# Performance work log

Measured on AMD Instinct MI355X. Metric: run time of the kernel, lower is better.

Reference implementation:

```python
import math
import jax, jax.numpy as jnp
import numpy as np

B, S, D, H = 2, 2048, 2048, 16
HD = D // H  # 128
EPS = 1e-5


def setup_inputs() -> dict:
    key = jax.random.key(0)
    ks = jax.random.split(key, 7)
    x = jax.random.normal(ks[0], (B, S, D), jnp.float32)
    # RoPE tables: (seqlen, head_dim//2)
    theta = 10000.0
    inv_freq = 1.0 / (theta ** (np.arange(0, HD, 2, dtype=np.float32) / HD))
    t = np.arange(S, dtype=np.float32)
    freqs = np.outer(t, inv_freq)  # (S, HD//2)
    freqs_cos = jnp.asarray(np.cos(freqs), jnp.float32)
    freqs_sin = jnp.asarray(np.sin(freqs), jnp.float32)
    sc = 0.02
    wq = jax.random.normal(ks[1], (D, D), jnp.float32) * sc  # stored (in, out)
    wk = jax.random.normal(ks[2], (D, D), jnp.float32) * sc
    wv = jax.random.normal(ks[3], (D, D), jnp.float32) * sc
    wu = jax.random.normal(ks[4], (D, D), jnp.float32) * sc
    wo = jax.random.normal(ks[5], (D, D), jnp.float32) * sc
    norm_w = jnp.ones((D,), jnp.float32)
    return {"x": x, "freqs_cos": freqs_cos, "freqs_sin": freqs_sin,
            "wq": wq, "wk": wk, "wv": wv, "wu": wu, "wo": wo, "norm_w": norm_w}


def _rope(t, cos, sin):
    # t: (B, S, H, HD); cos/sin: (S, HD//2)
    tr = t.reshape(t.shape[:-1] + (-1, 2))
    r, i = tr[..., 0], tr[..., 1]
    c = cos[None, :, None, :]
    s = sin[None, :, None, :]
    out_r = r * c - i * s
    out_i = r * s + i * c
    return jnp.stack([out_r, out_i], axis=-1).reshape(t.shape)


def reference(x, freqs_cos, freqs_sin, wq, wk, wv, wu, wo, norm_w):
    b, s, d = x.shape
    h = jax.nn.silu(x)  # pre-projection SiLU on the input
    q = (h @ wq).reshape(b, s, H, HD)
    k = (h @ wk).reshape(b, s, H, HD)
    v = (h @ wv).reshape(b, s, H, HD)
    u = h @ wu  # reshape->transpose->flatten in original is identity on (b,s,d)
    q = _rope(q, freqs_cos, freqs_sin)
    k = _rope(k, freqs_cos, freqs_sin)
    # scores: (b, H, s, s)
    scores = jnp.einsum('bqhd,bkhd->bhqk', q, k) / math.sqrt(HD)
    causal = jnp.tril(jnp.ones((s, s), bool))  # mask!=0 positions zeroed; silu(0)=0
    scores = jnp.where(causal[None, None], jax.nn.silu(scores), 0.0)
    out = jnp.einsum('bhqk,bkhd->bqhd', scores, v).reshape(b, s, d)
    # RMSNorm
    out = out * jax.lax.rsqrt(jnp.mean(out * out, axis=-1, keepdims=True) + EPS)
    out = out * norm_w
    out = out * u
    return out @ wo
```

## Files before the change

### kernel.cpp

```cpp
#include <hip/hip_runtime.h>
#include <hip/hip_bf16.h>
#include <cstdint>

typedef __attribute__((ext_vector_type(8))) short bf16x8;
typedef __attribute__((ext_vector_type(4))) float f32x4;
typedef unsigned short u16;

constexpr int B = 2, S = 2048, D = 2048, H = 16, HD = 128;
constexpr int M = B * S;
constexpr int NQKU = 6144;
constexpr int ATT_LD = 3072;
constexpr float SCALE = 0.08838834764831845f;

static __device__ __forceinline__ float b2f(u16 u) {
    union { float f; uint32_t i; } v; v.i = ((uint32_t)u) << 16; return v.f;
}
static __device__ __forceinline__ u16 f2b(float f) {
    union { float f; uint32_t i; } v; v.f = f;
    uint32_t x = v.i;
    return (u16)((x + 0x7FFFu + ((x >> 16) & 1u)) >> 16);
}

__device__ __forceinline__ void gll16(const void* g, void* l) {
    __builtin_amdgcn_global_load_lds(
        (const __attribute__((address_space(1))) uint32_t*)g,
        (__attribute__((address_space(3))) uint32_t*)l, 16, 0, 0);
}

#define BAR() do { asm volatile("" ::: "memory"); __builtin_amdgcn_s_barrier(); \
                   asm volatile("" ::: "memory"); } while (0)

__global__ __launch_bounds__(256) void silu_cast(const float* __restrict__ x,
                                                 u16* __restrict__ h, int n) {
    int i = (blockIdx.x * 256 + threadIdx.x) * 4;
    if (i >= n) return;
    float4 v = *(const float4*)(x + i);
    ushort4 o;
    o.x = f2b(v.x / (1.f + __expf(-v.x)));
    o.y = f2b(v.y / (1.f + __expf(-v.y)));
    o.z = f2b(v.z / (1.f + __expf(-v.z)));
    o.w = f2b(v.w / (1.f + __expf(-v.w)));
    *(ushort4*)(h + i) = o;
}

__global__ __launch_bounds__(256) void wcast(const float* __restrict__ w,
                                             u16* __restrict__ wT) {
    __shared__ float t[64][65];
    int tx = threadIdx.x & 63, ty = threadIdx.x >> 6;
    int kb = blockIdx.y * 64, nb = blockIdx.x * 64;
    for (int r = ty; r < 64; r += 4)
        t[r][tx] = w[(size_t)(kb + r) * D + nb + tx];
    __syncthreads();
    for (int r = ty; r < 64; r += 4)
        wT[(size_t)(nb + r) * D + kb + tx] = f2b(t[tx][r]);
}

__global__ __launch_bounds__(512, 2)
void gemm_qkuv(const u16* __restrict__ A, const u16* __restrict__ BT,
               u16* __restrict__ qku, u16* __restrict__ vt) {
    __shared__ u16 lds[65536];
    const int tid = threadIdx.x;
    const int lane = tid & 63, wid = tid >> 6;
    const int wm = wid >> 2, wn = wid & 3;
    const int l16 = lane & 15, lq = lane >> 4;

    const int orig = blockIdx.x;
    const int swz = (orig & 7) * 64 + (orig >> 3);
    const int mt = swz & 15, nt = swz >> 4;
    const int m0 = mt * 256, n0 = nt * 256;

    const int srow = tid >> 2;
    const int ce = ((tid & 3) * 8) ^ (((tid >> 5) & 1) << 4);
    const int rdx = (lq * 16) ^ (((l16 >> 3) & 1) << 5);

    const u16* As0 = A + (size_t)(m0 + srow) * D + ce;
    const u16* Bs0 = BT + (size_t)(n0 + srow) * D + ce;

    {
        u16* dA = lds + wid * 512;
        u16* dB = lds + 16384 + wid * 512;
        gll16(As0,                    dA);
        gll16(As0 + (size_t)128 * D,  dA + 8192);
        gll16(Bs0,                    dB);
        gll16(Bs0 + (size_t)128 * D,  dB + 8192);
        gll16(As0 + 32,                    dA + 4096);
        gll16(As0 + 32 + (size_t)128 * D,  dA + 8192 + 4096);
        gll16(Bs0 + 32,                    dB + 4096);
        gll16(Bs0 + 32 + (size_t)128 * D,  dB + 8192 + 4096);
    }
    asm volatile("s_waitcnt vmcnt(4)" ::: "memory");
    BAR();

    f32x4 acc[8][4] = {};
    bf16x8 a[8];
    const int rbB = (wn & 1) * 4096;

#define LOAD_A(kk)                                                            \
    _Pragma("unroll") for (int mi = 0; mi < 8; ++mi)                          \
        a[mi] = *(const bf16x8*)(Abase + (kk) * 8192 +                        \
                                 (mi * 16 + l16) * 64 + rdx);
#define LOAD_B(dst, nia, kk)                                                  \
    dst = *(const bf16x8*)(Bbase + (kk) * 8192 + rbB +                        \
                           ((nia) * 16 + l16) * 64 + rdx);
#define MFMA2(n0i, n1i)                                                       \
    __builtin_amdgcn_s_setprio(1);                                            \
    _Pragma("unroll") for (int mi = 0; mi < 8; ++mi) {                        \
        acc[mi][n0i] = __builtin_amdgcn_mfma_f32_16x16x32_bf16(a[mi], b0,     \
                            acc[mi][n0i], 0, 0, 0);                           \
        acc[mi][n1i] = __builtin_amdgcn_mfma_f32_16x16x32_bf16(a[mi], b1,     \
                            acc[mi][n1i], 0, 0, 0);                           \
    }                                                                          \
    __builtin_amdgcn_s_setprio(0);

    for (int kt = 0; kt < 32; ++kt) {
        const int buf = kt & 1;
        const char* Abase = (const char*)lds + buf * 65536 + wm * 16384;
        const char* Bbase = (const char*)lds + 32768 + buf * 65536 + (wn >> 1) * 16384;
        const bool st = (kt + 1) < 32;
        const u16* Asrc = As0 + (kt + 1) * 64;
        const u16* Bsrc = Bs0 + (kt + 1) * 64;
        u16* dA = lds + (buf ^ 1) * 32768 + wid * 512;
        u16* dB = dA + 16384;
        bf16x8 b0, b1;

        LOAD_A(0);
        LOAD_B(b0, 0, 0);
        LOAD_B(b1, 1, 0);
        if (st) { gll16(Asrc, dA); gll16(Asrc + (size_t)128 * D, dA + 8192); }
        BAR();
        MFMA2(0, 1);
        BAR();
        LOAD_B(b0, 2, 0);
        LOAD_B(b1, 3, 0);
        if (st) { gll16(Bsrc, dB); gll16(Bsrc + (size_t)128 * D, dB + 8192); }
        BAR();
        MFMA2(2, 3);
        if (kt == 31) asm volatile("s_waitcnt vmcnt(0)" ::: "memory");
        else         asm volatile("s_waitcnt vmcnt(4)" ::: "memory");
        BAR();
        LOAD_A(1);
        LOAD_B(b0, 0, 1);
        LOAD_B(b1, 1, 1);
        if (st) { gll16(Asrc + 32, dA + 4096); gll16(Asrc + 32 + (size_t)128 * D, dA + 8192 + 4096); }
        BAR();
        MFMA2(0, 1);
        BAR();
        LOAD_B(b0, 2, 1);
        LOAD_B(b1, 3, 1);
        if (st) { gll16(Bsrc + 32, dB + 4096); gll16(Bsrc + 32 + (size_t)128 * D, dB + 8192 + 4096); }
        BAR();
        MFMA2(2, 3);
        if (kt < 31) asm volatile("s_waitcnt vmcnt(4)" ::: "memory");
        BAR();
    }
#undef LOAD_A
#undef LOAD_B
#undef MFMA2

    if (n0 >= NQKU) {
#pragma unroll
        for (int mi = 0; mi < 8; ++mi)
#pragma unroll
            for (int ni = 0; ni < 4; ++ni) {
                int c = n0 - NQKU + wn * 64 + ni * 16 + l16;
                int hh = c >> 7, d = c & 127;
                int row0 = m0 + wm * 128 + mi * 16 + lq * 4;
                int bb = row0 >> 11, s0 = row0 & 2047;
                ushort4 pk = make_ushort4(f2b(acc[mi][ni][0]), f2b(acc[mi][ni][1]),
                                          f2b(acc[mi][ni][2]), f2b(acc[mi][ni][3]));
                *(ushort4*)(vt + (((size_t)(bb * H + hh) * HD + d) * S + s0)) = pk;
            }
    } else {
#pragma unroll
        for (int mi = 0; mi < 8; ++mi)
#pragma unroll
            for (int ni = 0; ni < 4; ++ni)
#pragma unroll
                for (int r = 0; r < 4; ++r) {
                    int row = m0 + wm * 128 + mi * 16 + lq * 4 + r;
                    int col = n0 + wn * 64 + ni * 16 + l16;
                    qku[(size_t)row * NQKU + col] = f2b(acc[mi][ni][r]);
                }
    }
}

__global__ __launch_bounds__(256)
void gemm_bt_f32(const u16* __restrict__ A, const u16* __restrict__ BT,
                 float* __restrict__ out, int lda, int ldc, int Kk) {
    __shared__ u16 As[128 * 32];
    __shared__ u16 Bs[128 * 32];
    const int tid = threadIdx.x;
    const int lane = tid & 63, w = tid >> 6;
    const int wm = w >> 1, wn = w & 1;
    const int l16 = lane & 15, lq = lane >> 4;
    const int m0 = blockIdx.y * 128, n0 = blockIdx.x * 128;
    const int rs = lane >> 2;
    const int cs = (lane & 3) * 8;
    f32x4 acc[4][4] = {};

    const u16* Ab = A + (size_t)(m0 + w * 32 + rs) * lda + cs;
    const u16* Bb = BT + (size_t)(n0 + w * 32 + rs) * Kk + cs;
    u16* Al = As + w * 32 * 32;
    u16* Bl = Bs + w * 32 * 32;

    for (int k0 = 0; k0 < Kk; k0 += 32) {
        gll16(Ab + k0, Al);
        gll16(Ab + k0 + (size_t)16 * lda, Al + 16 * 32);
        gll16(Bb + k0, Bl);
        gll16(Bb + k0 + (size_t)16 * Kk, Bl + 16 * 32);
        __syncthreads();
        bf16x8 af[4], bfr[4];
#pragma unroll
        for (int mi = 0; mi < 4; mi++)
            af[mi] = *(const bf16x8*)(As + (wm * 64 + mi * 16 + l16) * 32 + lq * 8);
#pragma unroll
        for (int ni = 0; ni < 4; ni++)
            bfr[ni] = *(const bf16x8*)(Bs + (wn * 64 + ni * 16 + l16) * 32 + lq * 8);
#pragma unroll
        for (int mi = 0; mi < 4; mi++)
#pragma unroll
            for (int ni = 0; ni < 4; ni++)
                acc[mi][ni] = __builtin_amdgcn_mfma_f32_16x16x32_bf16(
                    af[mi], bfr[ni], acc[mi][ni], 0, 0, 0);
        __syncthreads();
    }
#pragma unroll
    for (int mi = 0; mi < 4; mi++)
#pragma unroll
        for (int ni = 0; ni < 4; ni++)
#pragma unroll
            for (int r = 0; r < 4; r++) {
                int row = m0 + wm * 64 + mi * 16 + lq * 4 + r;
                int col = n0 + wn * 64 + ni * 16 + l16;
                out[(size_t)row * ldc + col] = acc[mi][ni][r];
            }
}

__global__ __launch_bounds__(256)
void reformat(const u16* __restrict__ qku, const float* __restrict__ fc,
              const float* __restrict__ fs, u16* __restrict__ qr,
              u16* __restrict__ kr) {
    int bh = blockIdx.x;
    int s0 = blockIdx.y * 64;
    int b = bh >> 4, h = bh & 15;
    int tid = threadIdx.x;
#pragma unroll
    for (int i = 0; i < 16; ++i) {
        int p = tid + i * 256;
        int row = p >> 6, pp = p & 63;
        int sgl = s0 + row;
        float c = fc[sgl * 64 + pp], sn = fs[sgl * 64 + pp];
        size_t src = (size_t)(b * S + sgl) * NQKU + h * HD + 2 * pp;
        size_t dst = ((size_t)bh * S + sgl) * HD + 2 * pp;
        {
            uint32_t qv = *(const uint32_t*)(qku + src);
            float r = b2f((u16)(qv & 0xffff)), im = b2f((u16)(qv >> 16));
            uint32_t o = (uint32_t)f2b(r * c - im * sn) |
                         ((uint32_t)f2b(r * sn + im * c) << 16);
            *(uint32_t*)(qr + dst) = o;
        }
        {
            uint32_t kv = *(const uint32_t*)(qku + src + 2048);
            float r = b2f((u16)(kv & 0xffff)), im = b2f((u16)(kv >> 16));
            uint32_t o = (uint32_t)f2b(r * c - im * sn) |
                         ((uint32_t)f2b(r * sn + im * c) << 16);
            *(uint32_t*)(kr + dst) = o;
        }
    }
}

__global__ __launch_bounds__(512, 2)
void hstu_attn(const u16* __restrict__ qr, const u16* __restrict__ kr,
               const u16* __restrict__ vt, float* __restrict__ att) {
    __shared__ u16 k_l[16384];
    __shared__ u16 v_l[16384];
    __shared__ u16 s_l[128 * 136];
    const int id = blockIdx.x;
    const int bh = (id & 7) * 4 + ((id >> 3) & 3);
    const int slot = id >> 5;
    const int b = bh >> 4, h = bh & 15;
    const int tid = threadIdx.x, lane = tid & 63, w = tid >> 6;
    const int l16 = lane & 15, lq = lane >> 4;
    const int wq = w >> 2, wk4 = w & 3;

    const u16* kb = kr + (size_t)bh * S * HD;
    const u16* vb = vt + (size_t)bh * HD * S;
    const int irow0 = tid >> 4, iu0 = tid & 15;

#define STAGE_K(k0_)                                                          \
    _Pragma("unroll") for (int r_ = 0; r_ < 4; ++r_) {                        \
        int row_ = irow0 + r_ * 32;                                           \
        int uc_ = iu0 ^ (row_ & 7);                                           \
        gll16(kb + (size_t)(k0_ + row_) * HD + uc_ * 8,                       \
              k_l + ((w * 64 + r_ * 512) << 3));                              \
    }
#define STAGE_V(k0_)                                                          \
    _Pragma("unroll") for (int r_ = 0; r_ < 4; ++r_) {                        \
        int row_ = irow0 + r_ * 32;                                           \
        int uc_ = iu0 ^ (row_ & 7);                                           \
        gll16(vb + (size_t)row_ * S + (k0_) + uc_ * 8,                        \
              v_l + ((w * 64 + r_ * 512) << 3));                              \
    }

    for (int pass = 0; pass < 2; ++pass) {
        const int t = pass ? (15 - slot) : slot;
        const int q0 = t * 128;

        bf16x8 qf[4][4];
#pragma unroll
        for (int mi = 0; mi < 4; ++mi)
#pragma unroll
            for (int kk = 0; kk < 4; ++kk)
                qf[mi][kk] = *(const bf16x8*)(qr +
                    ((size_t)bh * S + q0 + wq * 64 + mi * 16 + l16) * HD +
                    kk * 32 + lq * 8);
        f32x4 acco[4][2] = {};

        STAGE_K(0);
        STAGE_V(0);
        asm volatile("s_waitcnt vmcnt(0)" ::: "memory");
        BAR();

        for (int kt = 0; kt <= t; ++kt) {
            const int k0 = kt * 128;
            const bool st = kt < t;
            f32x4 accs[4][2] = {};
            __builtin_amdgcn_s_setprio(1);
#pragma unroll
            for (int kk = 0; kk < 4; ++kk)
#pragma unroll
                for (int ni = 0; ni < 2; ++ni) {
                    int row = wk4 * 32 + ni * 16 + l16;
                    bf16x8 kf = *(const bf16x8*)(k_l + row * 128 +
                                ((kk * 32 + lq * 8) ^ ((row & 7) << 3)));
#pragma unroll
                    for (int mi = 0; mi < 4; ++mi)
                        accs[mi][ni] = __builtin_amdgcn_mfma_f32_16x16x32_bf16(
                            qf[mi][kk], kf, accs[mi][ni], 0, 0, 0);
                }
            __builtin_amdgcn_s_setprio(0);
            const bool dg = (kt == t);
#pragma unroll
            for (int mi = 0; mi < 4; ++mi)
#pragma unroll
                for (int ni = 0; ni < 2; ++ni)
#pragma unroll
                    for (int r = 0; r < 4; ++r) {
                        int qrow = wq * 64 + mi * 16 + lq * 4 + r;
                        int krow = wk4 * 32 + ni * 16 + l16;
                        float vv = accs[mi][ni][r] * SCALE;
                        vv = (!dg || (k0 + krow <= q0 + qrow))
                                 ? vv * __builtin_amdgcn_rcpf(1.f + __expf(-vv))
                                 : 0.f;
                        s_l[qrow * 136 + krow] = f2b(vv);
                    }
            BAR();
            if (st) STAGE_K(k0 + 128);
            if (st) asm volatile("s_waitcnt vmcnt(4)" ::: "memory");
            else    asm volatile("s_waitcnt vmcnt(0)" ::: "memory");
            BAR();
            __builtin_amdgcn_s_setprio(1);
#pragma unroll
            for (int kk = 0; kk < 4; ++kk) {
                bf16x8 sf[4];
#pragma unroll
                for (int mi = 0; mi < 4; ++mi)
                    sf[mi] = *(const bf16x8*)(s_l + (wq * 64 + mi * 16 + l16) * 136 +
                                              kk * 32 + lq * 8);
#pragma unroll
                for (int ni = 0; ni < 2; ++ni) {
                    int row = wk4 * 32 + ni * 16 + l16;
                    bf16x8 vf = *(const bf16x8*)(v_l + row * 128 +
                                ((kk * 32 + lq * 8) ^ ((row & 7) << 3)));
#pragma unroll
                    for (int mi = 0; mi < 4; ++mi)
                        acco[mi][ni] = __builtin_amdgcn_mfma_f32_16x16x32_bf16(
                            sf[mi], vf, acco[mi][ni], 0, 0, 0);
                }
            }
            __builtin_amdgcn_s_setprio(0);
            BAR();
            if (st) {
                STAGE_V(k0 + 128);
                asm volatile("s_waitcnt vmcnt(4)" ::: "memory");
            }
            BAR();
        }
#pragma unroll
        for (int mi = 0; mi < 4; ++mi)
#pragma unroll
            for (int ni = 0; ni < 2; ++ni)
#pragma unroll
                for (int r = 0; r < 4; ++r)
                    att[(size_t)(b * S + q0 + wq * 64 + mi * 16 + lq * 4 + r) * ATT_LD +
                        h * HD + wk4 * 32 + ni * 16 + l16] = acco[mi][ni][r];
    }
#undef STAGE_K
#undef STAGE_V
}

__global__ __launch_bounds__(256)
void rms_mul(const float* __restrict__ att, u16* __restrict__ qku,
             const float* __restrict__ nw) {
    int row = blockIdx.x;
    int tid = threadIdx.x;
    const float* a = att + (size_t)row * ATT_LD + tid * 8;
    float4 v0 = *(const float4*)(a);
    float4 v1 = *(const float4*)(a + 4);
    float ss = v0.x * v0.x + v0.y * v0.y + v0.z * v0.z + v0.w * v0.w +
               v1.x * v1.x + v1.y * v1.y + v1.z * v1.z + v1.w * v1.w;
#pragma unroll
    for (int off = 32; off > 0; off >>= 1) ss += __shfl_down(ss, off, 64);
    __shared__ float red[4];
    int lane = tid & 63, w = tid >> 6;
    if (lane == 0) red[w] = ss;
    __syncthreads();
    float rs = rsqrtf((red[0] + red[1] + red[2] + red[3]) * (1.f / D) + 1e-5f);
    int col = tid * 8;
    u16* up = qku + (size_t)row * NQKU + 4096 + col;
    u16 ut[8];
    *(int4*)ut = *(const int4*)up;
    float f[8] = {v0.x, v0.y, v0.z, v0.w, v1.x, v1.y, v1.z, v1.w};
    u16 o[8];
#pragma unroll
    for (int j = 0; j < 8; j++)
        o[j] = f2b(f[j] * rs * nw[col + j] * b2f(ut[j]));
    *(int4*)up = *(int4*)o;
}

extern "C" void kernel_launch(void* const* d_in, const int* in_sizes, int n_in,
                              void* d_out, int out_size, void* d_ws, size_t ws_size,
                              hipStream_t stream) {
    const float* x  = (const float*)d_in[0];
    const float* fc = (const float*)d_in[1];
    const float* fs = (const float*)d_in[2];
    const float* wq = (const float*)d_in[3];
    const float* wk = (const float*)d_in[4];
    const float* wv = (const float*)d_in[5];
    const float* wu = (const float*)d_in[6];
    const float* wo = (const float*)d_in[7];
    const float* nw = (const float*)d_in[8];
    float* out = (float*)d_out;

    char* ws = (char*)d_ws;
    const size_t WSZ = (size_t)D * D * sizeof(u16);
    u16* h_b  = (u16*)(ws);
    u16* wT   = (u16*)(ws + 2 * WSZ);
    u16* qku  = (u16*)(ws + 7 * WSZ);
    u16* vt   = (u16*)(ws + 13 * WSZ);
    u16* k_r  = (u16*)(ws + 15 * WSZ);
    u16* q_r  = h_b;
    float* att = (float*)qku;

    silu_cast<<<M * D / 1024, 256, 0, stream>>>(x, h_b, M * D);
    dim3 wg(32, 32);
    wcast<<<wg, 256, 0, stream>>>(wq, wT + 0 * (size_t)D * D);
    wcast<<<wg, 256, 0, stream>>>(wk, wT + 1 * (size_t)D * D);
    wcast<<<wg, 256, 0, stream>>>(wu, wT + 2 * (size_t)D * D);
    wcast<<<wg, 256, 0, stream>>>(wv, wT + 3 * (size_t)D * D);
    wcast<<<wg, 256, 0, stream>>>(wo, wT + 4 * (size_t)D * D);

    gemm_qkuv<<<512, 512, 0, stream>>>(h_b, wT, qku, vt);

    reformat<<<dim3(32, 32), 256, 0, stream>>>(qku, fc, fs, q_r, k_r);
    hstu_attn<<<256, 512, 0, stream>>>(q_r, k_r, vt, att);
    rms_mul<<<M, 256, 0, stream>>>(att, qku, nw);
    gemm_bt_f32<<<dim3(D / 128, M / 128), 256, 0, stream>>>(
        qku + 4096, wT + 4 * (size_t)D * D, out, NQKU, D, D);
}
```

Measured before the change: 344.7 us.

## Process paired causal query tiles jointly in attention, sharing K/V tile loads

The attention kernel no longer runs the two query tiles (slot and 15-slot) in sequential passes. It interleaves them in a single key loop, so each staged K/V tile is loaded once and used by both tiles, with separate score buffers in shared memory. The output is now written as bf16 into the qku buffer, and rms_mul reads bf16 instead of fp32, which halves that intermediate traffic. The cost is more registers, with occupancy bounds lowered to one block per CU, more LDS, and an extra bf16 rounding before RMSNorm.

```diff
diff --git a/kernel.cpp b/kernel.cpp
--- a/kernel.cpp
+++ b/kernel.cpp
@@ -9,7 +9,6 @@
 constexpr int B = 2, S = 2048, D = 2048, H = 16, HD = 128;
 constexpr int M = B * S;
 constexpr int NQKU = 6144;
-constexpr int ATT_LD = 3072;
 constexpr float SCALE = 0.08838834764831845f;
 
 static __device__ __forceinline__ float b2f(u16 u) {
@@ -269,12 +268,13 @@
     }
 }
 
-__global__ __launch_bounds__(512, 2)
+__global__ __launch_bounds__(512, 1)
 void hstu_attn(const u16* __restrict__ qr, const u16* __restrict__ kr,
-               const u16* __restrict__ vt, float* __restrict__ att) {
+               const u16* __restrict__ vt, u16* __restrict__ attb) {
     __shared__ u16 k_l[16384];
     __shared__ u16 v_l[16384];
-    __shared__ u16 s_l[128 * 136];
+    __shared__ u16 s_A[128 * 136];
+    __shared__ u16 s_B[128 * 136];
     const int id = blockIdx.x;
     const int bh = (id & 7) * 4 + ((id >> 3) & 3);
     const int slot = id >> 5;
@@ -287,6 +287,9 @@
     const u16* vb = vt + (size_t)bh * HD * S;
     const int irow0 = tid >> 4, iu0 = tid & 15;
 
+    const int tA = slot, tB = 15 - slot;
+    const int qA = tA * 128, qB = tB * 128;
+
 #define STAGE_K(k0_)                                                          \
     _Pragma("unroll") for (int r_ = 0; r_ < 4; ++r_) {                        \
         int row_ = irow0 + r_ * 32;                                           \
@@ -301,114 +304,133 @@
         gll16(vb + (size_t)row_ * S + (k0_) + uc_ * 8,                        \
               v_l + ((w * 64 + r_ * 512) << 3));                              \
     }
-
-    for (int pass = 0; pass < 2; ++pass) {
-        const int t = pass ? (15 - slot) : slot;
-        const int q0 = t * 128;
-
-        bf16x8 qf[4][4];
-#pragma unroll
-        for (int mi = 0; mi < 4; ++mi)
-#pragma unroll
-            for (int kk = 0; kk < 4; ++kk)
-                qf[mi][kk] = *(const bf16x8*)(qr +
-                    ((size_t)bh * S + q0 + wq * 64 + mi * 16 + l16) * HD +
-                    kk * 32 + lq * 8);
-        f32x4 acco[4][2] = {};
-
-        STAGE_K(0);
-        STAGE_V(0);
-        asm volatile("s_waitcnt vmcnt(0)" ::: "memory");
-        BAR();
-
-        for (int kt = 0; kt <= t; ++kt) {
-            const int k0 = kt * 128;
-            const bool st = kt < t;
-            f32x4 accs[4][2] = {};
-            __builtin_amdgcn_s_setprio(1);
-#pragma unroll
-            for (int kk = 0; kk < 4; ++kk)
-#pragma unroll
-                for (int ni = 0; ni < 2; ++ni) {
-                    int row = wk4 * 32 + ni * 16 + l16;
-                    bf16x8 kf = *(const bf16x8*)(k_l + row * 128 +
-                                ((kk * 32 + lq * 8) ^ ((row & 7) << 3)));
+#define QK_TILE(qf_, s_x, q0_, tX_)                                           \
+    {                                                                          \
+        f32x4 accs[4][2] = {};                                                 \
+        __builtin_amdgcn_s_setprio(1);                                         \
+        _Pragma("unroll") for (int kk = 0; kk < 4; ++kk)                       \
+            _Pragma("unroll") for (int ni = 0; ni < 2; ++ni) {                 \
+                int row = wk4 * 32 + ni * 16 + l16;                            \
+                bf16x8 kf = *(const bf16x8*)(k_l + row * 128 +                 \
+                            ((kk * 32 + lq * 8) ^ ((row & 7) << 3)));          \
+                _Pragma("unroll") for (int mi = 0; mi < 4; ++mi)               \
+                    accs[mi][ni] = __builtin_amdgcn_mfma_f32_16x16x32_bf16(    \
+                        qf_[mi][kk], kf, accs[mi][ni], 0, 0, 0);               \
+            }                                                                  \
+        __builtin_amdgcn_s_setprio(0);                                         \
+        const bool dg_ = (kt == (tX_));                                        \
+        _Pragma("unroll") for (int mi = 0; mi < 4; ++mi)                       \
+            _Pragma("unroll") for (int ni = 0; ni < 2; ++ni)                   \
+                _Pragma("unroll") for (int r = 0; r < 4; ++r) {                \
+                    int qrow = wq * 64 + mi * 16 + lq * 4 + r;                 \
+                    int krow = wk4 * 32 + ni * 16 + l16;                       \
+                    float vv = accs[mi][ni][r] * SCALE;                        \
+                    vv = (!dg_ || (k0 + krow <= (q0_) + qrow))                 \
+                             ? vv * __builtin_amdgcn_rcpf(1.f + __expf(-vv))   \
+                             : 0.f;                                            \
+                    s_x[qrow * 136 + krow] = f2b(vv);                          \
+                }                                                              \
+    }
+
+    bf16x8 qfA[4][4], qfB[4][4];
+#pragma unroll
+    for (int mi = 0; mi < 4; ++mi)
+#pragma unroll
+        for (int kk = 0; kk < 4; ++kk) {
+            qfA[mi][kk] = *(const bf16x8*)(qr +
+                ((size_t)bh * S + qA + wq * 64 + mi * 16 + l16) * HD + kk * 32 + lq * 8);
+            qfB[mi][kk] = *(const bf16x8*)(qr +
+                ((size_t)bh * S + qB + wq * 64 + mi * 16 + l16) * HD + kk * 32 + lq * 8);
+        }
+    f32x4 accoA[4][2] = {}, accoB[4][2] = {};
+
+    STAGE_K(0);
+    STAGE_V(0);
+    asm volatile("s_waitcnt vmcnt(0)" ::: "memory");
+    BAR();
+
+    for (int kt = 0; kt <= tB; ++kt) {
+        const int k0 = kt * 128;
+        const bool aA = (kt <= tA);
+        const bool st = (kt < tB);
+
+        QK_TILE(qfB, s_B, qB, tB);
+        if (aA) QK_TILE(qfA, s_A, qA, tA);
+        BAR();
+        if (st) STAGE_K(k0 + 128);
+        if (st) asm volatile("s_waitcnt vmcnt(4)" ::: "memory");
+        else    asm volatile("s_waitcnt vmcnt(0)" ::: "memory");
+        BAR();
+        __builtin_amdgcn_s_setprio(1);
+#pragma unroll
+        for (int kk = 0; kk < 4; ++kk) {
+            bf16x8 vf[2];
+#pragma unroll
+            for (int ni = 0; ni < 2; ++ni) {
+                int row = wk4 * 32 + ni * 16 + l16;
+                vf[ni] = *(const bf16x8*)(v_l + row * 128 +
+                         ((kk * 32 + lq * 8) ^ ((row & 7) << 3)));
+            }
+            bf16x8 sf[4];
+#pragma unroll
+            for (int mi = 0; mi < 4; ++mi)
+                sf[mi] = *(const bf16x8*)(s_B + (wq * 64 + mi * 16 + l16) * 136 +
+                                          kk * 32 + lq * 8);
+#pragma unroll
+            for (int ni = 0; ni < 2; ++ni)
+#pragma unroll
+                for (int mi = 0; mi < 4; ++mi)
+                    accoB[mi][ni] = __builtin_amdgcn_mfma_f32_16x16x32_bf16(
+                        sf[mi], vf[ni], accoB[mi][ni], 0, 0, 0);
+            if (aA) {
+#pragma unroll
+                for (int mi = 0; mi < 4; ++mi)
+                    sf[mi] = *(const bf16x8*)(s_A + (wq * 64 + mi * 16 + l16) * 136 +
+                                              kk * 32 + lq * 8);
+#pragma unroll
+                for (int ni = 0; ni < 2; ++ni)
 #pragma unroll
                     for (int mi = 0; mi < 4; ++mi)
-                        accs[mi][ni] = __builtin_amdgcn_mfma_f32_16x16x32_bf16(
-                            qf[mi][kk], kf, accs[mi][ni], 0, 0, 0);
-                }
-            __builtin_amdgcn_s_setprio(0);
-            const bool dg = (kt == t);
-#pragma unroll
-            for (int mi = 0; mi < 4; ++mi)
-#pragma unroll
-                for (int ni = 0; ni < 2; ++ni)
-#pragma unroll
-                    for (int r = 0; r < 4; ++r) {
-                        int qrow = wq * 64 + mi * 16 + lq * 4 + r;
-                        int krow = wk4 * 32 + ni * 16 + l16;
-                        float vv = accs[mi][ni][r] * SCALE;
-                        vv = (!dg || (k0 + krow <= q0 + qrow))
-                                 ? vv * __builtin_amdgcn_rcpf(1.f + __expf(-vv))
-                                 : 0.f;
-                        s_l[qrow * 136 + krow] = f2b(vv);
-                    }
-            BAR();
-            if (st) STAGE_K(k0 + 128);
-            if (st) asm volatile("s_waitcnt vmcnt(4)" ::: "memory");
-            else    asm volatile("s_waitcnt vmcnt(0)" ::: "memory");
-            BAR();
-            __builtin_amdgcn_s_setprio(1);
-#pragma unroll
-            for (int kk = 0; kk < 4; ++kk) {
-                bf16x8 sf[4];
-#pragma unroll
-                for (int mi = 0; mi < 4; ++mi)
-                    sf[mi] = *(const bf16x8*)(s_l + (wq * 64 + mi * 16 + l16) * 136 +
-                                              kk * 32 + lq * 8);
-#pragma unroll
-                for (int ni = 0; ni < 2; ++ni) {
-                    int row = wk4 * 32 + ni * 16 + l16;
-                    bf16x8 vf = *(const bf16x8*)(v_l + row * 128 +
-                                ((kk * 32 + lq * 8) ^ ((row & 7) << 3)));
-#pragma unroll
-                    for (int mi = 0; mi < 4; ++mi)
-                        acco[mi][ni] = __builtin_amdgcn_mfma_f32_16x16x32_bf16(
-                            sf[mi], vf, acco[mi][ni], 0, 0, 0);
-                }
+                        accoA[mi][ni] = __builtin_amdgcn_mfma_f32_16x16x32_bf16(
+                            sf[mi], vf[ni], accoA[mi][ni], 0, 0, 0);
             }
-            __builtin_amdgcn_s_setprio(0);
-            BAR();
-            if (st) {
-                STAGE_V(k0 + 128);
-                asm volatile("s_waitcnt vmcnt(4)" ::: "memory");
+        }
+        __builtin_amdgcn_s_setprio(0);
+        BAR();
+        if (st) {
+            STAGE_V(k0 + 128);
+            asm volatile("s_waitcnt vmcnt(4)" ::: "memory");
+        }
+        BAR();
+    }
+#pragma unroll
+    for (int mi = 0; mi < 4; ++mi)
+#pragma unroll
+        for (int ni = 0; ni < 2; ++ni)
+#pragma unroll
+            for (int r = 0; r < 4; ++r) {
+                int col = h * HD + wk4 * 32 + ni * 16 + l16;
+                attb[(size_t)(b * S + qB + wq * 64 + mi * 16 + lq * 4 + r) * NQKU + col] =
+                    f2b(accoB[mi][ni][r]);
+                attb[(size_t)(b * S + qA + wq * 64 + mi * 16 + lq * 4 + r) * NQKU + col] =
+                    f2b(accoA[mi][ni][r]);
             }
-            BAR();
-        }
-#pragma unroll
-        for (int mi = 0; mi < 4; ++mi)
-#pragma unroll
-            for (int ni = 0; ni < 2; ++ni)
-#pragma unroll
-                for (int r = 0; r < 4; ++r)
-                    att[(size_t)(b * S + q0 + wq * 64 + mi * 16 + lq * 4 + r) * ATT_LD +
-                        h * HD + wk4 * 32 + ni * 16 + l16] = acco[mi][ni][r];
-    }
 #undef STAGE_K
 #undef STAGE_V
+#undef QK_TILE
 }
 
 __global__ __launch_bounds__(256)
-void rms_mul(const float* __restrict__ att, u16* __restrict__ qku,
-             const float* __restrict__ nw) {
+void rms_mul(u16* __restrict__ qku, const float* __restrict__ nw) {
     int row = blockIdx.x;
     int tid = threadIdx.x;
-    const float* a = att + (size_t)row * ATT_LD + tid * 8;
-    float4 v0 = *(const float4*)(a);
-    float4 v1 = *(const float4*)(a + 4);
-    float ss = v0.x * v0.x + v0.y * v0.y + v0.z * v0.z + v0.w * v0.w +
-               v1.x * v1.x + v1.y * v1.y + v1.z * v1.z + v1.w * v1.w;
+    int col = tid * 8;
+    u16 at[8];
+    *(int4*)at = *(const int4*)(qku + (size_t)row * NQKU + col);
+    float f[8];
+    float ss = 0.f;
+#pragma unroll
+    for (int j = 0; j < 8; j++) { f[j] = b2f(at[j]); ss += f[j] * f[j]; }
 #pragma unroll
     for (int off = 32; off > 0; off >>= 1) ss += __shfl_down(ss, off, 64);
     __shared__ float red[4];
@@ -416,11 +438,9 @@
     if (lane == 0) red[w] = ss;
     __syncthreads();
     float rs = rsqrtf((red[0] + red[1] + red[2] + red[3]) * (1.f / D) + 1e-5f);
-    int col = tid * 8;
     u16* up = qku + (size_t)row * NQKU + 4096 + col;
     u16 ut[8];
     *(int4*)ut = *(const int4*)up;
-    float f[8] = {v0.x, v0.y, v0.z, v0.w, v1.x, v1.y, v1.z, v1.w};
     u16 o[8];
 #pragma unroll
     for (int j = 0; j < 8; j++)
@@ -450,7 +470,6 @@
     u16* vt   = (u16*)(ws + 13 * WSZ);
     u16* k_r  = (u16*)(ws + 15 * WSZ);
     u16* q_r  = h_b;
-    float* att = (float*)qku;
 
     silu_cast<<<M * D / 1024, 256, 0, stream>>>(x, h_b, M * D);
     dim3 wg(32, 32);
@@ -463,8 +482,8 @@
     gemm_qkuv<<<512, 512, 0, stream>>>(h_b, wT, qku, vt);
 
     reformat<<<dim3(32, 32), 256, 0, stream>>>(qku, fc, fs, q_r, k_r);
-    hstu_attn<<<256, 512, 0, stream>>>(q_r, k_r, vt, att);
-    rms_mul<<<M, 256, 0, stream>>>(att, qku, nw);
+    hstu_attn<<<256, 512, 0, stream>>>(q_r, k_r, vt, qku);
+    rms_mul<<<M, 256, 0, stream>>>(qku, nw);
     gemm_bt_f32<<<dim3(D / 128, M / 128), 256, 0, stream>>>(
         qku + 4096, wT + 4 * (size_t)D * D, out, NQKU, D, D);
 }
```

Measured after the change: 365.0 us. 5.9% more time.

## Deepen QKUV GEMM prefetch and store attention output in bf16

Applied to the files above, without the earlier changes.

The QKUV GEMM now prefetches global-to-LDS loads further ahead. The second K-half of the next tile and the first half of the tile after it are issued while the current tile is computed, with the waitcnt thresholds raised to match. This is meant to hide more global load latency. Separately, the attention kernel writes its output as bf16 into the qku buffer instead of fp32, and rms_mul reads bf16. This halves attention write and norm read traffic at some precision cost before RMSNorm.

```diff
diff --git a/kernel.cpp b/kernel.cpp
--- a/kernel.cpp
+++ b/kernel.cpp
@@ -9,7 +9,6 @@
 constexpr int B = 2, S = 2048, D = 2048, H = 16, HD = 128;
 constexpr int M = B * S;
 constexpr int NQKU = 6144;
-constexpr int ATT_LD = 3072;
 constexpr float SCALE = 0.08838834764831845f;
 
 static __device__ __forceinline__ float b2f(u16 u) {
@@ -87,8 +86,14 @@
         gll16(As0 + 32 + (size_t)128 * D,  dA + 8192 + 4096);
         gll16(Bs0 + 32,                    dB + 4096);
         gll16(Bs0 + 32 + (size_t)128 * D,  dB + 8192 + 4096);
-    }
-    asm volatile("s_waitcnt vmcnt(4)" ::: "memory");
+        u16* dA1 = lds + 32768 + wid * 512;
+        u16* dB1 = lds + 32768 + 16384 + wid * 512;
+        gll16(As0 + 64,                    dA1);
+        gll16(As0 + 64 + (size_t)128 * D,  dA1 + 8192);
+        gll16(Bs0 + 64,                    dB1);
+        gll16(Bs0 + 64 + (size_t)128 * D,  dB1 + 8192);
+    }
+    asm volatile("s_waitcnt vmcnt(8)" ::: "memory");
     BAR();
 
     f32x4 acc[8][4] = {};
@@ -116,41 +121,49 @@
         const int buf = kt & 1;
         const char* Abase = (const char*)lds + buf * 65536 + wm * 16384;
         const char* Bbase = (const char*)lds + 32768 + buf * 65536 + (wn >> 1) * 16384;
-        const bool st = (kt + 1) < 32;
-        const u16* Asrc = As0 + (kt + 1) * 64;
-        const u16* Bsrc = Bs0 + (kt + 1) * 64;
-        u16* dA = lds + (buf ^ 1) * 32768 + wid * 512;
-        u16* dB = dA + 16384;
+        const bool st1 = (kt + 1) < 32;
+        const bool st2 = (kt + 2) < 32;
+        const u16* Asrc1 = As0 + (kt + 1) * 64;
+        const u16* Bsrc1 = Bs0 + (kt + 1) * 64;
+        const u16* Asrc2 = As0 + (kt + 2) * 64;
+        const u16* Bsrc2 = Bs0 + (kt + 2) * 64;
+        u16* dN = lds + (buf ^ 1) * 32768 + wid * 512;
+        u16* dC = lds + buf * 32768 + wid * 512;
         bf16x8 b0, b1;
 
         LOAD_A(0);
         LOAD_B(b0, 0, 0);
         LOAD_B(b1, 1, 0);
-        if (st) { gll16(Asrc, dA); gll16(Asrc + (size_t)128 * D, dA + 8192); }
+        if (st1) { gll16(Asrc1 + 32, dN + 4096);
+                   gll16(Asrc1 + 32 + (size_t)128 * D, dN + 8192 + 4096); }
         BAR();
         MFMA2(0, 1);
         BAR();
         LOAD_B(b0, 2, 0);
         LOAD_B(b1, 3, 0);
-        if (st) { gll16(Bsrc, dB); gll16(Bsrc + (size_t)128 * D, dB + 8192); }
+        if (st1) { gll16(Bsrc1 + 32, dN + 16384 + 4096);
+                   gll16(Bsrc1 + 32 + (size_t)128 * D, dN + 16384 + 8192 + 4096); }
         BAR();
         MFMA2(2, 3);
         if (kt == 31) asm volatile("s_waitcnt vmcnt(0)" ::: "memory");
-        else         asm volatile("s_waitcnt vmcnt(4)" ::: "memory");
+        else          asm volatile("s_waitcnt vmcnt(8)" ::: "memory");
         BAR();
         LOAD_A(1);
         LOAD_B(b0, 0, 1);
         LOAD_B(b1, 1, 1);
-        if (st) { gll16(Asrc + 32, dA + 4096); gll16(Asrc + 32 + (size_t)128 * D, dA + 8192 + 4096); }
+        if (st2) { gll16(Asrc2, dC);
+                   gll16(Asrc2 + (size_t)128 * D, dC + 8192); }
         BAR();
         MFMA2(0, 1);
         BAR();
         LOAD_B(b0, 2, 1);
         LOAD_B(b1, 3, 1);
-        if (st) { gll16(Bsrc + 32, dB + 4096); gll16(Bsrc + 32 + (size_t)128 * D, dB + 8192 + 4096); }
+        if (st2) { gll16(Bsrc2, dC + 16384);
+                   gll16(Bsrc2 + (size_t)128 * D, dC + 16384 + 8192); }
         BAR();
         MFMA2(2, 3);
-        if (kt < 31) asm volatile("s_waitcnt vmcnt(4)" ::: "memory");
+        if (kt < 30)       asm volatile("s_waitcnt vmcnt(8)" ::: "memory");
+        else if (kt == 30) asm volatile("s_waitcnt vmcnt(4)" ::: "memory");
         BAR();
     }
 #undef LOAD_A
@@ -271,7 +284,7 @@
 
 __global__ __launch_bounds__(512, 2)
 void hstu_attn(const u16* __restrict__ qr, const u16* __restrict__ kr,
-               const u16* __restrict__ vt, float* __restrict__ att) {
+               const u16* __restrict__ vt, u16* __restrict__ attb) {
     __shared__ u16 k_l[16384];
     __shared__ u16 v_l[16384];
     __shared__ u16 s_l[128 * 136];
@@ -392,23 +405,24 @@
             for (int ni = 0; ni < 2; ++ni)
 #pragma unroll
                 for (int r = 0; r < 4; ++r)
-                    att[(size_t)(b * S + q0 + wq * 64 + mi * 16 + lq * 4 + r) * ATT_LD +
-                        h * HD + wk4 * 32 + ni * 16 + l16] = acco[mi][ni][r];
+                    attb[(size_t)(b * S + q0 + wq * 64 + mi * 16 + lq * 4 + r) * NQKU +
+                         h * HD + wk4 * 32 + ni * 16 + l16] = f2b(acco[mi][ni][r]);
     }
 #undef STAGE_K
 #undef STAGE_V
 }
 
 __global__ __launch_bounds__(256)
-void rms_mul(const float* __restrict__ att, u16* __restrict__ qku,
-             const float* __restrict__ nw) {
+void rms_mul(u16* __restrict__ qku, const float* __restrict__ nw) {
     int row = blockIdx.x;
     int tid = threadIdx.x;
-    const float* a = att + (size_t)row * ATT_LD + tid * 8;
-    float4 v0 = *(const float4*)(a);
-    float4 v1 = *(const float4*)(a + 4);
-    float ss = v0.x * v0.x + v0.y * v0.y + v0.z * v0.z + v0.w * v0.w +
-               v1.x * v1.x + v1.y * v1.y + v1.z * v1.z + v1.w * v1.w;
+    int col = tid * 8;
+    u16 at[8];
+    *(int4*)at = *(const int4*)(qku + (size_t)row * NQKU + col);
+    float f[8];
+    float ss = 0.f;
+#pragma unroll
+    for (int j = 0; j < 8; j++) { f[j] = b2f(at[j]); ss += f[j] * f[j]; }
 #pragma unroll
     for (int off = 32; off > 0; off >>= 1) ss += __shfl_down(ss, off, 64);
     __shared__ float red[4];
@@ -416,11 +430,9 @@
     if (lane == 0) red[w] = ss;
     __syncthreads();
     float rs = rsqrtf((red[0] + red[1] + red[2] + red[3]) * (1.f / D) + 1e-5f);
-    int col = tid * 8;
     u16* up = qku + (size_t)row * NQKU + 4096 + col;
     u16 ut[8];
     *(int4*)ut = *(const int4*)up;
-    float f[8] = {v0.x, v0.y, v0.z, v0.w, v1.x, v1.y, v1.z, v1.w};
     u16 o[8];
 #pragma unroll
     for (int j = 0; j < 8; j++)
@@ -450,7 +462,6 @@
     u16* vt   = (u16*)(ws + 13 * WSZ);
     u16* k_r  = (u16*)(ws + 15 * WSZ);
     u16* q_r  = h_b;
-    float* att = (float*)qku;
 
     silu_cast<<<M * D / 1024, 256, 0, stream>>>(x, h_b, M * D);
     dim3 wg(32, 32);
@@ -463,8 +474,8 @@
     gemm_qkuv<<<512, 512, 0, stream>>>(h_b, wT, qku, vt);
 
     reformat<<<dim3(32, 32), 256, 0, stream>>>(qku, fc, fs, q_r, k_r);
-    hstu_attn<<<256, 512, 0, stream>>>(q_r, k_r, vt, att);
-    rms_mul<<<M, 256, 0, stream>>>(att, qku, nw);
+    hstu_attn<<<256, 512, 0, stream>>>(q_r, k_r, vt, qku);
+    rms_mul<<<M, 256, 0, stream>>>(qku, nw);
     gemm_bt_f32<<<dim3(D / 128, M / 128), 256, 0, stream>>>(
         qku + 4096, wT + 4 * (size_t)D * D, out, NQKU, D, D);
 }
```

Result: no change. 340.9 us (-1.1%).
